# Kernel optimization log

Hardware: AMD Instinct MI355X
Metric: run time of the kernel (lower is better)

Reference implementation:

```python
import jax, jax.numpy as jnp
import numpy as np

B, F, E, H, N = 50000, 128, 32, 2, 10


def setup_inputs() -> dict:
    key = jax.random.key(0)
    ks = jax.random.split(key, 12)
    return {
        "s_fts": jax.random.normal(ks[0], (B, F), jnp.float32),
        "t_fts": jax.random.normal(ks[1], (B, F), jnp.float32),
        "s_h_fts": jax.random.normal(ks[2], (B, H, F), jnp.float32),
        "t_h_fts": jax.random.normal(ks[3], (B, H, F), jnp.float32),
        "s_neg_fts": jax.random.normal(ks[4], (B, N, F), jnp.float32),
        "t_neg_fts": jax.random.normal(ks[5], (B, N, F), jnp.float32),
        "event_time": jax.random.uniform(ks[6], (B,), jnp.float32),
        "s_h_times": jax.random.uniform(ks[7], (B, H), jnp.float32),
        "t_h_times": jax.random.uniform(ks[8], (B, H), jnp.float32),
        "s_h_time_mask": jnp.ones((B, H), jnp.float32),
        "t_h_time_mask": jnp.ones((B, H), jnp.float32),
        "W_fts": jax.random.normal(ks[9], (F, E), jnp.float32) * 0.1,
        "b_fts": jax.random.normal(ks[10], (E,), jnp.float32) * 0.1,
        "a": jax.random.normal(ks[11], (2 * E, 1), jnp.float32) * 0.1,
        "delta_s": jnp.ones((1,), jnp.float32),
        "delta_t": jnp.ones((1,), jnp.float32),
    }


def _sqnorm(x):
    return jnp.sum(x * x, axis=-1)


def reference(s_fts, t_fts, s_h_fts, t_h_fts, s_neg_fts, t_neg_fts,
              event_time, s_h_times, t_h_times, s_h_time_mask, t_h_time_mask,
              W_fts, b_fts, a, delta_s, delta_t):
    emb = lambda x: x @ W_fts + b_fts  # fts2emb linear
    s_emb = emb(s_fts)                # [B,E]
    t_emb = emb(t_fts)                # [B,E]
    s_h_emb = emb(s_h_fts)            # [B,H,E]
    t_h_emb = emb(t_h_fts)            # [B,H,E]
    s_n_emb = emb(s_neg_fts)          # [B,N,E]
    t_n_emb = emb(t_neg_fts)          # [B,N,E]

    d_time_s = jnp.abs(event_time[:, None] - s_h_times)  # [B,H]
    d_time_t = jnp.abs(event_time[:, None] - t_h_times)  # [B,H]

    a_cur, a_his = a[:E, 0], a[E:, 0]
    # GAT-style score: [s_emb ; s_h_emb_i] @ a, vectorized over history slots
    score_s = (s_emb @ a_cur)[:, None] + s_h_emb @ a_his   # [B,H]
    score_t = (t_emb @ a_cur)[:, None] + t_h_emb @ a_his   # [B,H]
    sim_s = jax.nn.leaky_relu(jnp.exp(-delta_s * d_time_s) * score_s, 0.2)
    sim_t = jax.nn.leaky_relu(jnp.exp(-delta_t * d_time_t) * score_t, 0.2)
    att_s = jax.nn.softmax(sim_s, axis=1)  # [B,H]
    att_t = jax.nn.softmax(sim_t, axis=1)  # [B,H]

    # positive intensity
    p_mu = -_sqnorm(s_emb - t_emb)                               # [B]
    p_alpha_s = -_sqnorm(s_h_emb - t_emb[:, None, :])            # [B,H]
    w_s = att_s * jnp.exp(delta_s * d_time_s) * s_h_time_mask    # [B,H]
    w_t = att_t * jnp.exp(delta_t * d_time_t) * t_h_time_mask    # [B,H]
    p_lambda = p_mu + jnp.sum(w_s * p_alpha_s, axis=1)           # [B]

    # negative intensities via ||a-b||^2 = |a|^2 + |b|^2 - 2 a.b (avoids [B,H,N,E])
    n_mu_s = -(_sqnorm(s_emb)[:, None] + _sqnorm(t_n_emb)
               - 2.0 * jnp.einsum('be,bne->bn', s_emb, t_n_emb))      # [B,N]
    n_mu_t = -(_sqnorm(t_emb)[:, None] + _sqnorm(s_n_emb)
               - 2.0 * jnp.einsum('be,bne->bn', t_emb, s_n_emb))      # [B,N]
    n_alpha_s = -(_sqnorm(s_h_emb)[:, :, None] + _sqnorm(t_n_emb)[:, None, :]
                  - 2.0 * jnp.einsum('bhe,bne->bhn', s_h_emb, t_n_emb))  # [B,H,N]
    n_alpha_t = -(_sqnorm(t_h_emb)[:, :, None] + _sqnorm(s_n_emb)[:, None, :]
                  - 2.0 * jnp.einsum('bhe,bne->bhn', t_h_emb, s_n_emb))  # [B,H,N]
    n_lambda_s = n_mu_s + jnp.einsum('bh,bhn->bn', w_s, n_alpha_s)  # [B,N]
    n_lambda_t = n_mu_t + jnp.einsum('bh,bhn->bn', w_t, n_alpha_t)  # [B,N]

    return p_lambda, n_lambda_s, n_lambda_t
```

## Files before the change

### kernel.cpp

```cpp
#include <hip/hip_runtime.h>

typedef __attribute__((ext_vector_type(8))) short short8;
typedef __attribute__((ext_vector_type(4))) float f32x4;

constexpr int Fdim = 128;
constexpr int Edim = 32;
constexpr int NROW = 26;
constexpr int GB   = 16;

static __device__ inline short f2bf(float x) {
    union { float f; unsigned u; } v; v.f = x;
    unsigned r = v.u + 0x7fffu + ((v.u >> 16) & 1u);
    return (short)(r >> 16);
}

static __device__ inline const float* row_ptr(int r, int b,
    const float* __restrict__ s1, const float* __restrict__ t1,
    const float* __restrict__ sh, const float* __restrict__ th,
    const float* __restrict__ sn, const float* __restrict__ tn)
{
    if (r == 0) return s1 + (size_t)b * Fdim;
    if (r == 1) return t1 + (size_t)b * Fdim;
    if (r < 6) {
        int i = r - 2;
        const float* base = (i < 2) ? sh : th;
        return base + (size_t)b * (2 * Fdim) + (size_t)(i & 1) * Fdim;
    }
    int i = r - 6;
    const float* base = (i < 10) ? sn : tn;
    if (i >= 10) i -= 10;
    return base + (size_t)b * (10 * Fdim) + (size_t)i * Fdim;
}

__global__ __launch_bounds__(256) void mmdne_kernel(
    const float* __restrict__ s_fts,
    const float* __restrict__ t_fts,
    const float* __restrict__ s_h_fts,
    const float* __restrict__ t_h_fts,
    const float* __restrict__ s_neg,
    const float* __restrict__ t_neg,
    const float* __restrict__ ev_t,
    const float* __restrict__ s_h_times,
    const float* __restrict__ t_h_times,
    const float* __restrict__ s_mask,
    const float* __restrict__ t_mask,
    const float* __restrict__ Wg,
    const float* __restrict__ bft,
    const float* __restrict__ av,
    const float* __restrict__ dels,
    const float* __restrict__ delt,
    float* __restrict__ out,
    int nB)
{
    __shared__ float emb[NROW * GB * Edim];

    const int tid  = threadIdx.x;
    const int lane = tid & 63;
    const int wid  = tid >> 6;
    const int b0   = blockIdx.x * GB;
    const int nlo  = lane & 15;
    const int kg   = lane >> 4;

    {
        float* wl = emb;
        #pragma unroll
        for (int i = 0; i < 16; i++) wl[tid + 256 * i] = Wg[tid + 256 * i];
    }
    __syncthreads();

    short8 bf[2][4];
    #pragma unroll
    for (int nt = 0; nt < 2; nt++)
        #pragma unroll
        for (int kk = 0; kk < 4; kk++)
            #pragma unroll
            for (int j = 0; j < 8; j++)
                bf[nt][kk][j] = f2bf(emb[(kk * 32 + kg * 8 + j) * Edim + nt * 16 + nlo]);

    float bias_cb = 0.f;
    for (int j = 0; j < Edim; j++) bias_cb += bft[j] * (av[j] + av[Edim + j]);

    __syncthreads();

    for (int r = wid; r < NROW; r += 4) {
        const float* rp = row_ptr(r, b0 + nlo, s_fts, t_fts, s_h_fts, t_h_fts, s_neg, t_neg);
        f32x4 xa[8];
        #pragma unroll
        for (int kk = 0; kk < 4; kk++) {
            const float* p = rp + kk * 32 + kg * 8;
            xa[2 * kk]     = *(const f32x4*)p;
            xa[2 * kk + 1] = *(const f32x4*)(p + 4);
        }
        f32x4 acc0 = {0.f, 0.f, 0.f, 0.f};
        f32x4 acc1 = {0.f, 0.f, 0.f, 0.f};
        #pragma unroll
        for (int kk = 0; kk < 4; kk++) {
            short8 af;
            #pragma unroll
            for (int j = 0; j < 4; j++) af[j]     = f2bf(xa[2 * kk][j]);
            #pragma unroll
            for (int j = 0; j < 4; j++) af[4 + j] = f2bf(xa[2 * kk + 1][j]);
            acc0 = __builtin_amdgcn_mfma_f32_16x16x32_bf16(af, bf[0][kk], acc0, 0, 0, 0);
            acc1 = __builtin_amdgcn_mfma_f32_16x16x32_bf16(af, bf[1][kk], acc1, 0, 0, 0);
        }
        #pragma unroll
        for (int reg = 0; reg < 4; reg++) {
            const int bl = kg * 4 + reg;
            emb[r * (GB * Edim) + bl * Edim + nlo]      = acc0[reg];
            emb[r * (GB * Edim) + bl * Edim + 16 + nlo] = acc1[reg];
        }
    }
    __syncthreads();

    const int e    = lane & 31;
    const int half = lane >> 5;
    const float a_cur = av[e];
    const float a_his = av[Edim + e];
    const float dl    = half ? delt[0] : dels[0];

    #pragma unroll
    for (int i = 0; i < 4; i++) {
        const int bl = wid * 4 + i;
        const int b  = b0 + bl;

        float y[26];
        #pragma unroll
        for (int r = 0; r < 26; r++) y[r] = emb[r * (GB * Edim) + bl * Edim + e];

        float r0 = (half ? y[1] : y[0]) * a_cur;
        float r1 = (half ? y[4] : y[2]) * a_his;
        float r2 = (half ? y[5] : y[3]) * a_his;
        #pragma unroll
        for (int m = 1; m <= 16; m <<= 1) {
            r0 += __shfl_xor(r0, m);
            r1 += __shfl_xor(r1, m);
            r2 += __shfl_xor(r2, m);
        }

        const float et = ev_t[b];
        const float* htp = half ? t_h_times : s_h_times;
        const float* mkp = half ? t_mask : s_mask;
        const float h0t = htp[2 * b], h1t = htp[2 * b + 1];
        const float m0  = mkp[2 * b], m1  = mkp[2 * b + 1];
        const float d0 = fabsf(et - h0t), d1 = fabsf(et - h1t);
        const float sc0 = r0 + r1 + bias_cb, sc1 = r0 + r2 + bias_cb;
        float sim0 = expf(-dl * d0) * sc0; sim0 = sim0 >= 0.f ? sim0 : 0.2f * sim0;
        float sim1 = expf(-dl * d1) * sc1; sim1 = sim1 >= 0.f ? sim1 : 0.2f * sim1;
        const float mx = fmaxf(sim0, sim1);
        const float p0 = expf(sim0 - mx), p1 = expf(sim1 - mx);
        const float inv = 1.f / (p0 + p1);
        const float w0_ = p0 * inv * expf(dl * d0) * m0;
        const float w1_ = p1 * inv * expf(dl * d1) * m1;

        {
            float q0 = y[0] - y[1]; q0 *= q0;
            float q1 = y[2] - y[1]; q1 *= q1;
            float q2 = y[3] - y[1]; q2 *= q2;
            float comb = q0 + w0_ * q1 + w1_ * q2;
            #pragma unroll
            for (int m = 1; m <= 16; m <<= 1) comb += __shfl_xor(comb, m);
            if (lane == 0) out[b] = -comb;
        }

        float* onS = out + nB + (size_t)b * 10;
        float* onT = out + nB + (size_t)nB * 10 + (size_t)b * 10;
        const float Aa = half ? y[1] : y[0];
        const float Ha = half ? y[4] : y[2];
        const float Hb = half ? y[5] : y[3];
        #pragma unroll
        for (int n = 0; n < 10; n++) {
            const float cn = half ? y[6 + n] : y[16 + n];
            float u  = Aa - cn; u  *= u;
            float v0 = Ha - cn; v0 *= v0;
            float v1 = Hb - cn; v1 *= v1;
            float comb = u + w0_ * v0 + w1_ * v1;
            #pragma unroll
            for (int m = 1; m <= 16; m <<= 1) comb += __shfl_xor(comb, m);
            if (lane == n)      onS[n] = -comb;
            if (lane == 32 + n) onT[n] = -comb;
        }
    }
}

extern "C" void kernel_launch(void* const* d_in, const int* in_sizes, int n_in,
                              void* d_out, int out_size, void* d_ws, size_t ws_size,
                              hipStream_t stream) {
    const float* s_fts     = (const float*)d_in[0];
    const float* t_fts     = (const float*)d_in[1];
    const float* s_h_fts   = (const float*)d_in[2];
    const float* t_h_fts   = (const float*)d_in[3];
    const float* s_neg     = (const float*)d_in[4];
    const float* t_neg     = (const float*)d_in[5];
    const float* ev_t      = (const float*)d_in[6];
    const float* s_h_times = (const float*)d_in[7];
    const float* t_h_times = (const float*)d_in[8];
    const float* s_mask    = (const float*)d_in[9];
    const float* t_mask    = (const float*)d_in[10];
    const float* Wg        = (const float*)d_in[11];
    const float* bft       = (const float*)d_in[12];
    const float* av        = (const float*)d_in[13];
    const float* dels      = (const float*)d_in[14];
    const float* delt      = (const float*)d_in[15];

    const int nB = in_sizes[6];
    const int blocks = (nB + GB - 1) / GB;

    mmdne_kernel<<<blocks, 256, 0, stream>>>(
        s_fts, t_fts, s_h_fts, t_h_fts, s_neg, t_neg, ev_t,
        s_h_times, t_h_times, s_mask, t_mask, Wg, bft, av, dels, delt,
        (float*)d_out, nB);
}
```

Measured before the change: 624.3 us.

## Fold negative-sample distances into MFMA epilogue via expanded squared norms

The weighted sum of squared distances to each negative is expanded algebraically into per-batch constants (sum of w|x|^2, sum of w·x, sum of w). The negative-row embeddings are therefore consumed straight from the MFMA accumulators and never written to LDS. This shrinks the shared-memory footprint, adds an XOR swizzle to LDS indexing, prefetches the next row's global loads during compute, uses packed bf16 conversion, and raises occupancy through launch bounds. The risk is extra shuffles per output and a change in floating-point rounding from the expanded form.

```diff
diff --git a/kernel.cpp b/kernel.cpp
--- a/kernel.cpp
+++ b/kernel.cpp
@@ -5,13 +5,22 @@
 
 constexpr int Fdim = 128;
 constexpr int Edim = 32;
-constexpr int NROW = 26;
 constexpr int GB   = 16;
+
+constexpr int KP_BASE = 3072;
+constexpr int SB_BASE = 5120;
+constexpr int ARENA_F = 5152;
 
 static __device__ inline short f2bf(float x) {
     union { float f; unsigned u; } v; v.f = x;
     unsigned r = v.u + 0x7fffu + ((v.u >> 16) & 1u);
     return (short)(r >> 16);
+}
+
+static __device__ __forceinline__ unsigned cvt2(float lo, float hi) {
+    unsigned r;
+    asm("v_cvt_pk_bf16_f32 %0, %1, %2" : "=v"(r) : "v"(lo), "v"(hi));
+    return r;
 }
 
 static __device__ inline const float* row_ptr(int r, int b,
@@ -32,7 +41,28 @@
     return base + (size_t)b * (10 * Fdim) + (size_t)i * Fdim;
 }
 
-__global__ __launch_bounds__(256) void mmdne_kernel(
+static __device__ __forceinline__ void load_row(f32x4 (&xa)[8], const float* rp, int kg) {
+    #pragma unroll
+    for (int kk = 0; kk < 4; kk++) {
+        const float* p = rp + kk * 32 + kg * 8;
+        xa[2 * kk]     = *(const f32x4*)p;
+        xa[2 * kk + 1] = *(const f32x4*)(p + 4);
+    }
+}
+
+static __device__ __forceinline__ void conv_row(short8 (&afk)[4], const f32x4 (&xa)[8]) {
+    #pragma unroll
+    for (int kk = 0; kk < 4; kk++) {
+        union { unsigned u[4]; short8 s; } A;
+        A.u[0] = cvt2(xa[2 * kk][0],     xa[2 * kk][1]);
+        A.u[1] = cvt2(xa[2 * kk][2],     xa[2 * kk][3]);
+        A.u[2] = cvt2(xa[2 * kk + 1][0], xa[2 * kk + 1][1]);
+        A.u[3] = cvt2(xa[2 * kk + 1][2], xa[2 * kk + 1][3]);
+        afk[kk] = A.s;
+    }
+}
+
+__global__ __launch_bounds__(256, 4) void mmdne_kernel(
     const float* __restrict__ s_fts,
     const float* __restrict__ t_fts,
     const float* __restrict__ s_h_fts,
@@ -52,7 +82,7 @@
     float* __restrict__ out,
     int nB)
 {
-    __shared__ float emb[NROW * GB * Edim];
+    __shared__ float arena[ARENA_F];
 
     const int tid  = threadIdx.x;
     const int lane = tid & 63;
@@ -62,9 +92,8 @@
     const int kg   = lane >> 4;
 
     {
-        float* wl = emb;
-        #pragma unroll
-        for (int i = 0; i < 16; i++) wl[tid + 256 * i] = Wg[tid + 256 * i];
+        #pragma unroll
+        for (int i = 0; i < 16; i++) arena[tid + 256 * i] = Wg[tid + 256 * i];
     }
     __syncthreads();
 
@@ -75,109 +104,132 @@
         for (int kk = 0; kk < 4; kk++)
             #pragma unroll
             for (int j = 0; j < 8; j++)
-                bf[nt][kk][j] = f2bf(emb[(kk * 32 + kg * 8 + j) * Edim + nt * 16 + nlo]);
+                bf[nt][kk][j] = f2bf(arena[(kk * 32 + kg * 8 + j) * Edim + nt * 16 + nlo]);
 
     float bias_cb = 0.f;
     for (int j = 0; j < Edim; j++) bias_cb += bft[j] * (av[j] + av[Edim + j]);
 
     __syncthreads();
 
-    for (int r = wid; r < NROW; r += 4) {
+    for (int r = wid; r < 6; r += 4) {
         const float* rp = row_ptr(r, b0 + nlo, s_fts, t_fts, s_h_fts, t_h_fts, s_neg, t_neg);
-        f32x4 xa[8];
+        f32x4 xa[8]; load_row(xa, rp, kg);
+        short8 afk[4]; conv_row(afk, xa);
+        f32x4 a0 = {0.f,0.f,0.f,0.f}, a1 = {0.f,0.f,0.f,0.f};
         #pragma unroll
         for (int kk = 0; kk < 4; kk++) {
-            const float* p = rp + kk * 32 + kg * 8;
-            xa[2 * kk]     = *(const f32x4*)p;
-            xa[2 * kk + 1] = *(const f32x4*)(p + 4);
-        }
-        f32x4 acc0 = {0.f, 0.f, 0.f, 0.f};
-        f32x4 acc1 = {0.f, 0.f, 0.f, 0.f};
-        #pragma unroll
-        for (int kk = 0; kk < 4; kk++) {
-            short8 af;
-            #pragma unroll
-            for (int j = 0; j < 4; j++) af[j]     = f2bf(xa[2 * kk][j]);
-            #pragma unroll
-            for (int j = 0; j < 4; j++) af[4 + j] = f2bf(xa[2 * kk + 1][j]);
-            acc0 = __builtin_amdgcn_mfma_f32_16x16x32_bf16(af, bf[0][kk], acc0, 0, 0, 0);
-            acc1 = __builtin_amdgcn_mfma_f32_16x16x32_bf16(af, bf[1][kk], acc1, 0, 0, 0);
+            a0 = __builtin_amdgcn_mfma_f32_16x16x32_bf16(afk[kk], bf[0][kk], a0, 0, 0, 0);
+            a1 = __builtin_amdgcn_mfma_f32_16x16x32_bf16(afk[kk], bf[1][kk], a1, 0, 0, 0);
         }
         #pragma unroll
         for (int reg = 0; reg < 4; reg++) {
             const int bl = kg * 4 + reg;
-            emb[r * (GB * Edim) + bl * Edim + nlo]      = acc0[reg];
-            emb[r * (GB * Edim) + bl * Edim + 16 + nlo] = acc1[reg];
-        }
-    }
-    __syncthreads();
-
-    const int e    = lane & 31;
-    const int half = lane >> 5;
-    const float a_cur = av[e];
-    const float a_his = av[Edim + e];
-    const float dl    = half ? delt[0] : dels[0];
-
-    #pragma unroll
-    for (int i = 0; i < 4; i++) {
-        const int bl = wid * 4 + i;
-        const int b  = b0 + bl;
-
-        float y[26];
-        #pragma unroll
-        for (int r = 0; r < 26; r++) y[r] = emb[r * (GB * Edim) + bl * Edim + e];
-
-        float r0 = (half ? y[1] : y[0]) * a_cur;
-        float r1 = (half ? y[4] : y[2]) * a_his;
-        float r2 = (half ? y[5] : y[3]) * a_his;
-        #pragma unroll
-        for (int m = 1; m <= 16; m <<= 1) {
-            r0 += __shfl_xor(r0, m);
-            r1 += __shfl_xor(r1, m);
-            r2 += __shfl_xor(r2, m);
-        }
-
-        const float et = ev_t[b];
-        const float* htp = half ? t_h_times : s_h_times;
-        const float* mkp = half ? t_mask : s_mask;
-        const float h0t = htp[2 * b], h1t = htp[2 * b + 1];
-        const float m0  = mkp[2 * b], m1  = mkp[2 * b + 1];
-        const float d0 = fabsf(et - h0t), d1 = fabsf(et - h1t);
-        const float sc0 = r0 + r1 + bias_cb, sc1 = r0 + r2 + bias_cb;
-        float sim0 = expf(-dl * d0) * sc0; sim0 = sim0 >= 0.f ? sim0 : 0.2f * sim0;
-        float sim1 = expf(-dl * d1) * sc1; sim1 = sim1 >= 0.f ? sim1 : 0.2f * sim1;
-        const float mx = fmaxf(sim0, sim1);
-        const float p0 = expf(sim0 - mx), p1 = expf(sim1 - mx);
-        const float inv = 1.f / (p0 + p1);
-        const float w0_ = p0 * inv * expf(dl * d0) * m0;
-        const float w1_ = p1 * inv * expf(dl * d1) * m1;
-
-        {
-            float q0 = y[0] - y[1]; q0 *= q0;
-            float q1 = y[2] - y[1]; q1 *= q1;
-            float q2 = y[3] - y[1]; q2 *= q2;
-            float comb = q0 + w0_ * q1 + w1_ * q2;
-            #pragma unroll
-            for (int m = 1; m <= 16; m <<= 1) comb += __shfl_xor(comb, m);
-            if (lane == 0) out[b] = -comb;
-        }
-
-        float* onS = out + nB + (size_t)b * 10;
-        float* onT = out + nB + (size_t)nB * 10 + (size_t)b * 10;
-        const float Aa = half ? y[1] : y[0];
-        const float Ha = half ? y[4] : y[2];
-        const float Hb = half ? y[5] : y[3];
-        #pragma unroll
-        for (int n = 0; n < 10; n++) {
-            const float cn = half ? y[6 + n] : y[16 + n];
-            float u  = Aa - cn; u  *= u;
-            float v0 = Ha - cn; v0 *= v0;
-            float v1 = Hb - cn; v1 *= v1;
-            float comb = u + w0_ * v0 + w1_ * v1;
-            #pragma unroll
-            for (int m = 1; m <= 16; m <<= 1) comb += __shfl_xor(comb, m);
-            if (lane == n)      onS[n] = -comb;
-            if (lane == 32 + n) onT[n] = -comb;
+            arena[r * 512 + bl * 32 + (nlo ^ (kg << 3))]        = a0[reg];
+            arena[r * 512 + bl * 32 + ((nlo + 16) ^ (kg << 3))] = a1[reg];
+        }
+    }
+    __syncthreads();
+
+    {
+        const int e    = lane & 31;
+        const int half = lane >> 5;
+        const float a_cur = av[e];
+        const float a_his = av[Edim + e];
+        const float dl    = half ? delt[0] : dels[0];
+        float2* kp = (float2*)(arena + KP_BASE);
+
+        #pragma unroll
+        for (int i = 0; i < 4; i++) {
+            const int bl = wid * 4 + i;
+            const int b  = b0 + bl;
+            const int swz = (bl >> 2) << 3;
+
+            float y[6];
+            #pragma unroll
+            for (int r = 0; r < 6; r++) y[r] = arena[r * 512 + bl * 32 + (e ^ swz)];
+
+            float r0 = (half ? y[1] : y[0]) * a_cur;
+            float r1 = (half ? y[4] : y[2]) * a_his;
+            float r2 = (half ? y[5] : y[3]) * a_his;
+            #pragma unroll
+            for (int m = 1; m <= 16; m <<= 1) {
+                r0 += __shfl_xor(r0, m);
+                r1 += __shfl_xor(r1, m);
+                r2 += __shfl_xor(r2, m);
+            }
+
+            const float et = ev_t[b];
+            const float* htp = half ? t_h_times : s_h_times;
+            const float* mkp = half ? t_mask : s_mask;
+            const float h0t = htp[2 * b], h1t = htp[2 * b + 1];
+            const float m0  = mkp[2 * b], m1  = mkp[2 * b + 1];
+            const float d0 = fabsf(et - h0t), d1 = fabsf(et - h1t);
+            const float sc0 = r0 + r1 + bias_cb, sc1 = r0 + r2 + bias_cb;
+            float sim0 = expf(-dl * d0) * sc0; sim0 = sim0 >= 0.f ? sim0 : 0.2f * sim0;
+            float sim1 = expf(-dl * d1) * sc1; sim1 = sim1 >= 0.f ? sim1 : 0.2f * sim1;
+            const float mx = fmaxf(sim0, sim1);
+            const float p0 = expf(sim0 - mx), p1 = expf(sim1 - mx);
+            const float inv = 1.f / (p0 + p1);
+            const float w0_ = p0 * inv * expf(dl * d0) * m0;
+            const float w1_ = p1 * inv * expf(dl * d1) * m1;
+
+            {
+                float q0 = y[0] - y[1]; q0 *= q0;
+                float q1 = y[2] - y[1]; q1 *= q1;
+                float q2 = y[3] - y[1]; q2 *= q2;
+                float comb = q0 + w0_ * q1 + w1_ * q2;
+                #pragma unroll
+                for (int m = 1; m <= 16; m <<= 1) comb += __shfl_xor(comb, m);
+                if (lane == 0) out[b] = -comb;
+            }
+
+            const float A_  = half ? y[1] : y[0];
+            const float H0_ = half ? y[4] : y[2];
+            const float H1_ = half ? y[5] : y[3];
+            const float k_  = A_ * A_ + w0_ * H0_ * H0_ + w1_ * H1_ * H1_;
+            const float p_  = A_ + w0_ * H0_ + w1_ * H1_;
+            kp[half * 512 + bl * 32 + (e ^ swz)] = make_float2(k_, p_);
+            if (e == 0) arena[SB_BASE + half * 16 + bl] = 1.f + w0_ + w1_;
+        }
+    }
+    __syncthreads();
+
+    {
+        const float2* kp = (const float2*)(arena + KP_BASE);
+        f32x4 xa[8];
+        int r = 6 + wid;
+        load_row(xa, row_ptr(r, b0 + nlo, s_fts, t_fts, s_h_fts, t_h_fts, s_neg, t_neg), kg);
+        for (; r < 26; r += 4) {
+            short8 afk[4];
+            conv_row(afk, xa);
+            if (r + 4 < 26)
+                load_row(xa, row_ptr(r + 4, b0 + nlo, s_fts, t_fts, s_h_fts, t_h_fts, s_neg, t_neg), kg);
+
+            f32x4 a0 = {0.f,0.f,0.f,0.f}, a1 = {0.f,0.f,0.f,0.f};
+            #pragma unroll
+            for (int kk = 0; kk < 4; kk++) {
+                a0 = __builtin_amdgcn_mfma_f32_16x16x32_bf16(afk[kk], bf[0][kk], a0, 0, 0, 0);
+                a1 = __builtin_amdgcn_mfma_f32_16x16x32_bf16(afk[kk], bf[1][kk], a1, 0, 0, 0);
+            }
+
+            const int sideH = (r < 16) ? 1 : 0;
+            const int n     = (r < 16) ? (r - 6) : (r - 16);
+            float* on = out + nB + (r < 16 ? (size_t)nB * 10 : (size_t)0);
+
+            #pragma unroll
+            for (int reg = 0; reg < 4; reg++) {
+                const int bl = kg * 4 + reg;
+                const float2 kp0 = kp[sideH * 512 + bl * 32 + (nlo ^ (kg << 3))];
+                const float2 kp1 = kp[sideH * 512 + bl * 32 + ((nlo + 16) ^ (kg << 3))];
+                const float S    = arena[SB_BASE + sideH * 16 + bl];
+                const float q0 = a0[reg], q1 = a1[reg];
+                float part = (kp0.x + kp1.x)
+                           - 2.f * (q0 * kp0.y + q1 * kp1.y)
+                           + S * (q0 * q0 + q1 * q1);
+                #pragma unroll
+                for (int m = 1; m <= 8; m <<= 1) part += __shfl_xor(part, m);
+                if (nlo == reg) on[(size_t)(b0 + bl) * 10 + n] = -part;
+            }
         }
     }
 }
```

Result: no change. 612.9 us (-1.8%).
